# Kernel tuning notes

Measured on AMD Instinct MI355X. Metric: run time of the kernel, lower is better.

## Reference

```python
import jax, jax.numpy as jnp
import numpy as np

B, P, E, H = 32, 16, 50000, 128
EPS = 1e-5


def setup_inputs() -> dict:
    key = jax.random.key(0)
    ks = jax.random.split(key, 8)
    return {
        "inputs": jax.random.randint(ks[0], (B, P, E), 0, 2, dtype=jnp.int32),
        "emb": jax.random.normal(ks[1], (E, H), jnp.float32) * 0.02,
        "w1": jax.random.normal(ks[2], (H, H), jnp.float32) / np.sqrt(H),
        "b1": jax.random.normal(ks[3], (H,), jnp.float32) * 0.01,
        "w2": jax.random.normal(ks[4], (H, H), jnp.float32) / np.sqrt(H),
        "b2": jax.random.normal(ks[5], (H,), jnp.float32) * 0.01,
        "ln1_g": jnp.ones((H,), jnp.float32),
        "ln1_b": jnp.zeros((H,), jnp.float32),
        "ln2_g": jnp.ones((H,), jnp.float32),
        "ln2_b": jnp.zeros((H,), jnp.float32),
        "bn1_g": jnp.ones((H,), jnp.float32),
        "bn1_b": jnp.zeros((H,), jnp.float32),
        "bn2_g": jnp.ones((H,), jnp.float32),
        "bn2_b": jnp.zeros((H,), jnp.float32),
    }


def _layer_norm(x, g, b):
    mu = x.mean(-1, keepdims=True)
    var = ((x - mu) ** 2).mean(-1, keepdims=True)
    return g * (x - mu) / jnp.sqrt(var + EPS) + b


def _batch_norm_eval(x, g, b):
    # eval-mode BatchNorm1d with running_mean=0, running_var=1
    return g * x / jnp.sqrt(1.0 + EPS) + b


def reference(inputs, emb, w1, b1, w2, b2, ln1_g, ln1_b, ln2_g, ln2_b,
              bn1_g, bn1_b, bn2_g, bn2_b):
    # padding_idx=0: embedding row 0 is zero (but still counted in the mean,
    # matching the torch loop which averages over all selected indices)
    emb0 = emb.at[0].set(0.0)
    mask = (inputs == 1).astype(emb.dtype)            # [B, P, E] multi-hot
    sums = jnp.einsum("bpe,eh->bph", mask, emb0)       # segment-sum as one GEMM
    cnt = mask.sum(-1, keepdims=True)                  # [B, P, 1]
    path_emb = jnp.where(cnt > 0, sums / jnp.maximum(cnt, 1.0), 0.0)
    x = path_emb.mean(axis=1)                          # mean over paths -> [B, H]
    x = _layer_norm(x, ln1_g, ln1_b)
    x = jax.nn.relu(x @ w1.T + b1)
    x = _batch_norm_eval(x, bn1_g, bn1_b)              # dropout = identity (eval)
    x = _layer_norm(x, ln2_g, ln2_b)
    x = jax.nn.relu(x @ w2.T + b2)
    x = _batch_norm_eval(x, bn2_g, bn2_b)
    return x
```

## Files before the change

### kernel.cpp

```cpp
#include <hip/hip_runtime.h>
#include <stdint.h>

#define E_DIM 50000
#define EP2   50176
#define HD    128
#define BD    32
#define PD    16
#define MD    512
#define KCHUNK 448
#define NKC   112
#define NST   7
#define NEB   784
#define EPSF  1e-5f

typedef short short8 __attribute__((ext_vector_type(8)));
typedef float f32x4  __attribute__((ext_vector_type(4)));

__device__ __forceinline__ uint16_t f2bf(float f) {
  uint32_t u = __float_as_uint(f);
  u += 0x7FFFu + ((u >> 16) & 1u);
  return (uint16_t)(u >> 16);
}

__global__ __launch_bounds__(256) void k_prep(const float* __restrict__ emb,
                                              const int* __restrict__ inp,
                                              uint16_t* __restrict__ embF,
                                              uint8_t* __restrict__ bitsT,
                                              float* __restrict__ cnt) {
  __shared__ __align__(16) uint16_t lds[HD * 64];
  __shared__ int sc[4];
  const int t = threadIdx.x;

  if (blockIdx.x < NEB) {
    const int e0 = blockIdx.x * 64;
#pragma unroll
    for (int pass = 0; pass < 8; ++pass) {
      const int el = pass * 8 + (t >> 5);
      const int h  = (t & 31) * 4;
      const int eg = e0 + el;
      float4 v = {0.f, 0.f, 0.f, 0.f};
      if (eg < E_DIM && eg != 0)
        v = *(const float4*)(emb + (size_t)eg * HD + h);
      const uint16_t q0 = f2bf(v.x), q1 = f2bf(v.y), q2 = f2bf(v.z), q3 = f2bf(v.w);
      lds[(h + 0) * 64 + (el ^ (((h + 0) & 7) << 3))] = q0;
      lds[(h + 1) * 64 + (el ^ (((h + 1) & 7) << 3))] = q1;
      lds[(h + 2) * 64 + (el ^ (((h + 2) & 7) << 3))] = q2;
      lds[(h + 3) * 64 + (el ^ (((h + 3) & 7) << 3))] = q3;
    }
    __syncthreads();
    const int w    = t >> 6;
    const int lane = t & 63;
    const int r16  = lane & 15;
    const int kgq  = (lane >> 4) * 8;
    uint16_t* outp = embF + (size_t)blockIdx.x * 8192 + lane * 8;
#pragma unroll
    for (int fr = 0; fr < 4; ++fr) {
      const int f  = w * 4 + fr;
      const int h  = (f & 7) * 16 + r16;
      const int el = (f >> 3) * 32 + kgq;
      short8 d = *(const short8*)(lds + h * 64 + (el ^ ((h & 7) << 3)));
      *(short8*)(outp + f * 512) = d;
    }
  } else {
    const int r = blockIdx.x - NEB;
    const int* rp = inp + (size_t)r * E_DIM;
    int c = 0;
#pragma unroll 3
    for (int i = 0; i < 24; ++i) {
      const int idx = i * 2048 + t * 8;
      const int4 v0 = *(const int4*)(rp + idx);
      const int4 v1 = *(const int4*)(rp + idx + 4);
      const uint32_t b = (uint32_t)(v0.x == 1)        | ((uint32_t)(v0.y == 1) << 1)
                       | ((uint32_t)(v0.z == 1) << 2) | ((uint32_t)(v0.w == 1) << 3)
                       | ((uint32_t)(v1.x == 1) << 4) | ((uint32_t)(v1.y == 1) << 5)
                       | ((uint32_t)(v1.z == 1) << 6) | ((uint32_t)(v1.w == 1) << 7);
      c += __popc(b);
      const int c0 = i * 256 + t;
      bitsT[(size_t)(c0 / 56) * 28672 + r * 56 + (c0 % 56)] = (uint8_t)b;
    }
    if (t < 106) {
      const int idx = 49152 + t * 8;
      const int4 v0 = *(const int4*)(rp + idx);
      const int4 v1 = *(const int4*)(rp + idx + 4);
      const uint32_t b = (uint32_t)(v0.x == 1)        | ((uint32_t)(v0.y == 1) << 1)
                       | ((uint32_t)(v0.z == 1) << 2) | ((uint32_t)(v0.w == 1) << 3)
                       | ((uint32_t)(v1.x == 1) << 4) | ((uint32_t)(v1.y == 1) << 5)
                       | ((uint32_t)(v1.z == 1) << 6) | ((uint32_t)(v1.w == 1) << 7);
      c += __popc(b);
      const int c0 = 6144 + t;
      bitsT[(size_t)(c0 / 56) * 28672 + r * 56 + (c0 % 56)] = (uint8_t)b;
    } else if (t < 128) {
      const int c0 = 6144 + t;
      bitsT[(size_t)(c0 / 56) * 28672 + r * 56 + (c0 % 56)] = 0;
    }
#pragma unroll
    for (int o = 1; o < 64; o <<= 1) c += __shfl_xor(c, o);
    if ((t & 63) == 0) sc[t >> 6] = c;
    __syncthreads();
    if (t == 0) cnt[r] = (float)(sc[0] + sc[1] + sc[2] + sc[3]);
  }
}

__global__ __launch_bounds__(512, 4) void k_gemm(const uint8_t* __restrict__ bitsT,
                                                 const uint16_t* __restrict__ embF,
                                                 uint16_t* __restrict__ part) {
  __shared__ __align__(16) uint8_t lds[57344];

  const int t    = threadIdx.x;
  const int lane = t & 63;
  const int w    = t >> 6;
  const int kc   = blockIdx.x >> 2;
  const int ch   = blockIdx.x & 3;

  {
    const char* eb = (const char*)embF + (size_t)kc * 114688;
    const char* ab = (const char*)bitsT + (size_t)kc * 28672;
#define BADDR(IDX) (eb + ((IDX) >> 8) * 16384 + ((((IDX) >> 7) & 1) * 8192) \
                       + ((ch * 2 + (((IDX) >> 6) & 1)) * 1024) + ((IDX) & 63) * 16)
    uint4 b0, b1, b2, b3, a0, a1, a2, a3;
    b0 = *(const uint4*)BADDR(t);
    b1 = *(const uint4*)BADDR(512 + t);
    b2 = *(const uint4*)BADDR(1024 + t);
    a0 = *(const uint4*)(ab + t * 16);
    a1 = *(const uint4*)(ab + (512 + t) * 16);
    a2 = *(const uint4*)(ab + (1024 + t) * 16);
    if (t < 256) {
      b3 = *(const uint4*)BADDR(1536 + t);
      a3 = *(const uint4*)(ab + (1536 + t) * 16);
    }
    *(uint4*)(lds + t * 16)                  = b0;
    *(uint4*)(lds + (512 + t) * 16)          = b1;
    *(uint4*)(lds + (1024 + t) * 16)         = b2;
    *(uint4*)(lds + 28672 + t * 16)          = a0;
    *(uint4*)(lds + 28672 + (512 + t) * 16)  = a1;
    *(uint4*)(lds + 28672 + (1024 + t) * 16) = a2;
    if (t < 256) {
      *(uint4*)(lds + (1536 + t) * 16)          = b3;
      *(uint4*)(lds + 28672 + (1536 + t) * 16)  = a3;
    }
#undef BADDR
  }
  __syncthreads();

  const int r16 = lane & 15;
  const int g4  = lane >> 4;
  const int abase = 28672 + (w * 64 + r16) * 56 + g4;
  const int bbase = lane * 16;

  f32x4 acc[4][2];
#pragma unroll
  for (int rg = 0; rg < 4; ++rg)
#pragma unroll
    for (int cg = 0; cg < 2; ++cg) acc[rg][cg] = (f32x4){0.f, 0.f, 0.f, 0.f};

#define UNPACK(DST, B)                                            \
  {                                                               \
    union { uint32_t u[4]; short8 s; } x_;                        \
    x_.u[0] = ((B) & 1u) * 0x3F80u        + ((B) & 2u) * 0x1FC00000u;   \
    x_.u[1] = (((B) >> 2) & 1u) * 0x3F80u + (((B) >> 2) & 2u) * 0x1FC00000u; \
    x_.u[2] = (((B) >> 4) & 1u) * 0x3F80u + (((B) >> 4) & 2u) * 0x1FC00000u; \
    x_.u[3] = (((B) >> 6) & 1u) * 0x3F80u + (((B) >> 6) & 2u) * 0x1FC00000u; \
    DST = x_.s;                                                   \
  }

#pragma unroll
  for (int s = 0; s < NST; ++s) {
    short8 bf[2][2];
#pragma unroll
    for (int ks = 0; ks < 2; ++ks)
#pragma unroll
      for (int cg = 0; cg < 2; ++cg)
        bf[ks][cg] = *(const short8*)(lds + s * 4096 + ks * 2048 + cg * 1024 + bbase);
#pragma unroll
    for (int rg = 0; rg < 4; ++rg) {
#pragma unroll
      for (int ks = 0; ks < 2; ++ks) {
        const uint32_t b = lds[abase + rg * 896 + s * 8 + ks * 4];
        short8 af;
        UNPACK(af, b)
        acc[rg][0] = __builtin_amdgcn_mfma_f32_16x16x32_bf16(af, bf[ks][0], acc[rg][0], 0, 0, 0);
        acc[rg][1] = __builtin_amdgcn_mfma_f32_16x16x32_bf16(af, bf[ks][1], acc[rg][1], 0, 0, 0);
      }
    }
  }
#undef UNPACK

  const int jr = (lane >> 4) << 2;
#pragma unroll
  for (int rg = 0; rg < 4; ++rg)
#pragma unroll
    for (int cg = 0; cg < 2; ++cg) {
      uint16_t* pt = part + (size_t)kc * (MD * HD)
                   + (size_t)(w * 64 + rg * 16 + jr) * HD + ch * 32 + cg * 16 + r16;
#pragma unroll
      for (int j = 0; j < 4; ++j)
        pt[j * HD] = f2bf(acc[rg][cg][j]);
    }
}

__global__ __launch_bounds__(512) void k_reduce(const uint16_t* __restrict__ part,
                                                const float* __restrict__ cnt,
                                                float* __restrict__ pe) {
  __shared__ float red[512];
  const int r   = blockIdx.x;
  const int t   = threadIdx.x;
  const int col = t & 127;
  const int sub = t >> 7;
  const uint16_t* pp = part + (size_t)(sub * 28) * (MD * HD) + (size_t)r * HD + col;
  float s = 0.f;
#pragma unroll
  for (int i = 0; i < 28; ++i)
    s += __uint_as_float((uint32_t)pp[(size_t)i * (MD * HD)] << 16);
  red[t] = s;
  __syncthreads();
  if (t < 128) {
    const float tot = red[t] + red[t + 128] + red[t + 256] + red[t + 384];
    const float c   = cnt[r];
    pe[r * HD + t] = (c > 0.f) ? (tot / c) : 0.f;
  }
}

__global__ __launch_bounds__(128) void k_tail(
    const float* __restrict__ pe,
    const float* __restrict__ w1, const float* __restrict__ b1,
    const float* __restrict__ w2, const float* __restrict__ b2,
    const float* __restrict__ ln1g, const float* __restrict__ ln1b,
    const float* __restrict__ ln2g, const float* __restrict__ ln2b,
    const float* __restrict__ bn1g, const float* __restrict__ bn1b,
    const float* __restrict__ bn2g, const float* __restrict__ bn2b,
    float* __restrict__ out) {
  const int b = blockIdx.x, t = threadIdx.x;
  __shared__ float sh[HD];
  __shared__ float red[HD];

  float x = 0.f;
#pragma unroll
  for (int p = 0; p < PD; ++p) x += pe[(b * PD + p) * HD + t];
  x *= (1.f / PD);

  const float bninv = rsqrtf(1.f + EPSF);

  red[t] = x; __syncthreads();
  for (int o = 64; o > 0; o >>= 1) { if (t < o) red[t] += red[t + o]; __syncthreads(); }
  const float mu1 = red[0] * (1.f / HD); __syncthreads();
  const float d1 = x - mu1;
  red[t] = d1 * d1; __syncthreads();
  for (int o = 64; o > 0; o >>= 1) { if (t < o) red[t] += red[t + o]; __syncthreads(); }
  const float v1 = red[0] * (1.f / HD); __syncthreads();
  const float y1 = ln1g[t] * d1 * rsqrtf(v1 + EPSF) + ln1b[t];

  sh[t] = y1; __syncthreads();
  float a = b1[t];
  const float4* wrow1 = (const float4*)(w1 + (size_t)t * HD);
#pragma unroll 8
  for (int k = 0; k < 32; ++k) {
    const float4 w = wrow1[k];
    a += w.x * sh[k * 4] + w.y * sh[k * 4 + 1] + w.z * sh[k * 4 + 2] + w.w * sh[k * 4 + 3];
  }
  a = fmaxf(a, 0.f);
  a = bn1g[t] * a * bninv + bn1b[t];
  __syncthreads();

  red[t] = a; __syncthreads();
  for (int o = 64; o > 0; o >>= 1) { if (t < o) red[t] += red[t + o]; __syncthreads(); }
  const float mu2 = red[0] * (1.f / HD); __syncthreads();
  const float d2 = a - mu2;
  red[t] = d2 * d2; __syncthreads();
  for (int o = 64; o > 0; o >>= 1) { if (t < o) red[t] += red[t + o]; __syncthreads(); }
  const float v2 = red[0] * (1.f / HD); __syncthreads();
  const float y2 = ln2g[t] * d2 * rsqrtf(v2 + EPSF) + ln2b[t];

  sh[t] = y2; __syncthreads();
  float a2 = b2[t];
  const float4* wrow2 = (const float4*)(w2 + (size_t)t * HD);
#pragma unroll 8
  for (int k = 0; k < 32; ++k) {
    const float4 w = wrow2[k];
    a2 += w.x * sh[k * 4] + w.y * sh[k * 4 + 1] + w.z * sh[k * 4 + 2] + w.w * sh[k * 4 + 3];
  }
  a2 = fmaxf(a2, 0.f);
  a2 = bn2g[t] * a2 * bninv + bn2b[t];
  out[b * HD + t] = a2;
}

extern "C" void kernel_launch(void* const* d_in, const int* in_sizes, int n_in,
                              void* d_out, int out_size, void* d_ws, size_t ws_size,
                              hipStream_t stream) {
  const int*   inp  = (const int*)d_in[0];
  const float* emb  = (const float*)d_in[1];
  const float* w1   = (const float*)d_in[2];
  const float* b1   = (const float*)d_in[3];
  const float* w2   = (const float*)d_in[4];
  const float* b2   = (const float*)d_in[5];
  const float* ln1g = (const float*)d_in[6];
  const float* ln1b = (const float*)d_in[7];
  const float* ln2g = (const float*)d_in[8];
  const float* ln2b = (const float*)d_in[9];
  const float* bn1g = (const float*)d_in[10];
  const float* bn1b = (const float*)d_in[11];
  const float* bn2g = (const float*)d_in[12];
  const float* bn2b = (const float*)d_in[13];
  float* out = (float*)d_out;

  char* ws = (char*)d_ws;
  uint8_t*  bitsT = (uint8_t*)ws;
  uint16_t* embF  = (uint16_t*)(ws + 3211328);
  uint16_t* part  = (uint16_t*)(ws + 3211328 + 12845056);
  float*    cnt   = (float*)(ws + 3211328 + 12845056 + 14680064);
  float*    pe    = (float*)(ws + 3211328 + 12845056 + 14680064 + 2048);

  k_prep<<<NEB + MD, 256, 0, stream>>>(emb, inp, embF, bitsT, cnt);
  k_gemm<<<NKC * 4, 512, 0, stream>>>(bitsT, embF, part);
  k_reduce<<<MD, 512, 0, stream>>>(part, cnt, pe);
  k_tail<<<BD, 128, 0, stream>>>(pe, w1, b1, w2, b2, ln1g, ln1b, ln2g, ln2b,
                                 bn1g, bn1b, bn2g, bn2b, out);
}
```

Baseline: 61.95 us.

## Fuse prep, GEMM, reduce and tail into one cooperative persistent kernel

Replaces the four separate launches with one cooperative kernel of 256 blocks. The prep, split-K GEMM and reduce/tail phases are separated by grid-wide syncs, and each block handles several prep and GEMM units. The reduce kernel is folded into the tail, so each of 32 blocks sums all K-chunk partials for its 16 rows and no pe buffer is written. The aim is to remove launch gaps and a global round trip, at the cost of grid-sync overhead, fewer blocks in flight, and a serial 112-chunk reduction on only 32 blocks. A fallback to three regular launches covers the case where the cooperative launch fails.

Result: slower. 168.7 us (+172.4%).

```diff
diff --git a/kernel.cpp b/kernel.cpp
--- a/kernel.cpp
+++ b/kernel.cpp
@@ -1,5 +1,8 @@
 #include <hip/hip_runtime.h>
+#include <hip/hip_cooperative_groups.h>
 #include <stdint.h>
+
+namespace cg = cooperative_groups;
 
 #define E_DIM 50000
 #define EP2   50176
@@ -7,10 +10,10 @@
 #define BD    32
 #define PD    16
 #define MD    512
-#define KCHUNK 448
 #define NKC   112
 #define NST   7
 #define NEB   784
+#define GRID  256
 #define EPSF  1e-5f
 
 typedef short short8 __attribute__((ext_vector_type(8)));
@@ -22,95 +25,83 @@
   return (uint16_t)(u >> 16);
 }
 
-__global__ __launch_bounds__(256) void k_prep(const float* __restrict__ emb,
-                                              const int* __restrict__ inp,
-                                              uint16_t* __restrict__ embF,
-                                              uint8_t* __restrict__ bitsT,
-                                              float* __restrict__ cnt) {
-  __shared__ __align__(16) uint16_t lds[HD * 64];
-  __shared__ int sc[4];
-  const int t = threadIdx.x;
-
-  if (blockIdx.x < NEB) {
-    const int e0 = blockIdx.x * 64;
-#pragma unroll
-    for (int pass = 0; pass < 8; ++pass) {
-      const int el = pass * 8 + (t >> 5);
-      const int h  = (t & 31) * 4;
-      const int eg = e0 + el;
-      float4 v = {0.f, 0.f, 0.f, 0.f};
-      if (eg < E_DIM && eg != 0)
-        v = *(const float4*)(emb + (size_t)eg * HD + h);
-      const uint16_t q0 = f2bf(v.x), q1 = f2bf(v.y), q2 = f2bf(v.z), q3 = f2bf(v.w);
-      lds[(h + 0) * 64 + (el ^ (((h + 0) & 7) << 3))] = q0;
-      lds[(h + 1) * 64 + (el ^ (((h + 1) & 7) << 3))] = q1;
-      lds[(h + 2) * 64 + (el ^ (((h + 2) & 7) << 3))] = q2;
-      lds[(h + 3) * 64 + (el ^ (((h + 3) & 7) << 3))] = q3;
-    }
-    __syncthreads();
-    const int w    = t >> 6;
-    const int lane = t & 63;
-    const int r16  = lane & 15;
-    const int kgq  = (lane >> 4) * 8;
-    uint16_t* outp = embF + (size_t)blockIdx.x * 8192 + lane * 8;
-#pragma unroll
-    for (int fr = 0; fr < 4; ++fr) {
-      const int f  = w * 4 + fr;
-      const int h  = (f & 7) * 16 + r16;
-      const int el = (f >> 3) * 32 + kgq;
-      short8 d = *(const short8*)(lds + h * 64 + (el ^ ((h & 7) << 3)));
-      *(short8*)(outp + f * 512) = d;
-    }
-  } else {
-    const int r = blockIdx.x - NEB;
-    const int* rp = inp + (size_t)r * E_DIM;
-    int c = 0;
+
+__device__ __forceinline__ void embF_load(const float* __restrict__ emb,
+                                          int unit, int tt, uint16_t* tl) {
+#pragma unroll
+  for (int pass = 0; pass < 8; ++pass) {
+    const int el = pass * 8 + (tt >> 5);
+    const int h  = (tt & 31) * 4;
+    const int eg = unit * 64 + el;
+    float4 v = {0.f, 0.f, 0.f, 0.f};
+    if (eg < E_DIM && eg != 0)
+      v = *(const float4*)(emb + (size_t)eg * HD + h);
+    const uint16_t q0 = f2bf(v.x), q1 = f2bf(v.y), q2 = f2bf(v.z), q3 = f2bf(v.w);
+    tl[(h + 0) * 64 + (el ^ (((h + 0) & 7) << 3))] = q0;
+    tl[(h + 1) * 64 + (el ^ (((h + 1) & 7) << 3))] = q1;
+    tl[(h + 2) * 64 + (el ^ (((h + 2) & 7) << 3))] = q2;
+    tl[(h + 3) * 64 + (el ^ (((h + 3) & 7) << 3))] = q3;
+  }
+}
+__device__ __forceinline__ void embF_store(uint16_t* __restrict__ embF,
+                                           int unit, int tt, const uint16_t* tl) {
+  const int w = tt >> 6, lane = tt & 63;
+  const int r16 = lane & 15, kgq = (lane >> 4) * 8;
+  uint16_t* outp = embF + (size_t)unit * 8192 + lane * 8;
+#pragma unroll
+  for (int fr = 0; fr < 4; ++fr) {
+    const int f  = w * 4 + fr;
+    const int h  = (f & 7) * 16 + r16;
+    const int el = (f >> 3) * 32 + kgq;
+    short8 d = *(const short8*)(tl + h * 64 + (el ^ ((h & 7) << 3)));
+    *(short8*)(outp + f * 512) = d;
+  }
+}
+
+__device__ __forceinline__ int bitpack_row(const int* __restrict__ inp,
+                                           uint8_t* __restrict__ bitsT,
+                                           int r, int t) {
+  const int* rp = inp + (size_t)r * E_DIM;
+  int c = 0;
 #pragma unroll 3
-    for (int i = 0; i < 24; ++i) {
-      const int idx = i * 2048 + t * 8;
-      const int4 v0 = *(const int4*)(rp + idx);
-      const int4 v1 = *(const int4*)(rp + idx + 4);
-      const uint32_t b = (uint32_t)(v0.x == 1)        | ((uint32_t)(v0.y == 1) << 1)
-                       | ((uint32_t)(v0.z == 1) << 2) | ((uint32_t)(v0.w == 1) << 3)
-                       | ((uint32_t)(v1.x == 1) << 4) | ((uint32_t)(v1.y == 1) << 5)
-                       | ((uint32_t)(v1.z == 1) << 6) | ((uint32_t)(v1.w == 1) << 7);
-      c += __popc(b);
-      const int c0 = i * 256 + t;
-      bitsT[(size_t)(c0 / 56) * 28672 + r * 56 + (c0 % 56)] = (uint8_t)b;
-    }
-    if (t < 106) {
-      const int idx = 49152 + t * 8;
-      const int4 v0 = *(const int4*)(rp + idx);
-      const int4 v1 = *(const int4*)(rp + idx + 4);
-      const uint32_t b = (uint32_t)(v0.x == 1)        | ((uint32_t)(v0.y == 1) << 1)
-                       | ((uint32_t)(v0.z == 1) << 2) | ((uint32_t)(v0.w == 1) << 3)
-                       | ((uint32_t)(v1.x == 1) << 4) | ((uint32_t)(v1.y == 1) << 5)
-                       | ((uint32_t)(v1.z == 1) << 6) | ((uint32_t)(v1.w == 1) << 7);
-      c += __popc(b);
-      const int c0 = 6144 + t;
-      bitsT[(size_t)(c0 / 56) * 28672 + r * 56 + (c0 % 56)] = (uint8_t)b;
-    } else if (t < 128) {
-      const int c0 = 6144 + t;
-      bitsT[(size_t)(c0 / 56) * 28672 + r * 56 + (c0 % 56)] = 0;
-    }
-#pragma unroll
-    for (int o = 1; o < 64; o <<= 1) c += __shfl_xor(c, o);
-    if ((t & 63) == 0) sc[t >> 6] = c;
-    __syncthreads();
-    if (t == 0) cnt[r] = (float)(sc[0] + sc[1] + sc[2] + sc[3]);
-  }
-}
-
-__global__ __launch_bounds__(512, 4) void k_gemm(const uint8_t* __restrict__ bitsT,
-                                                 const uint16_t* __restrict__ embF,
-                                                 uint16_t* __restrict__ part) {
-  __shared__ __align__(16) uint8_t lds[57344];
-
-  const int t    = threadIdx.x;
+  for (int i = 0; i < 12; ++i) {
+    const int idx = i * 4096 + t * 8;
+    const int4 v0 = *(const int4*)(rp + idx);
+    const int4 v1 = *(const int4*)(rp + idx + 4);
+    const uint32_t b = (uint32_t)(v0.x == 1)        | ((uint32_t)(v0.y == 1) << 1)
+                     | ((uint32_t)(v0.z == 1) << 2) | ((uint32_t)(v0.w == 1) << 3)
+                     | ((uint32_t)(v1.x == 1) << 4) | ((uint32_t)(v1.y == 1) << 5)
+                     | ((uint32_t)(v1.z == 1) << 6) | ((uint32_t)(v1.w == 1) << 7);
+    c += __popc(b);
+    const int c0 = i * 512 + t;
+    bitsT[(size_t)(c0 / 56) * 28672 + r * 56 + (c0 % 56)] = (uint8_t)b;
+  }
+  if (t < 106) {
+    const int idx = 49152 + t * 8;
+    const int4 v0 = *(const int4*)(rp + idx);
+    const int4 v1 = *(const int4*)(rp + idx + 4);
+    const uint32_t b = (uint32_t)(v0.x == 1)        | ((uint32_t)(v0.y == 1) << 1)
+                     | ((uint32_t)(v0.z == 1) << 2) | ((uint32_t)(v0.w == 1) << 3)
+                     | ((uint32_t)(v1.x == 1) << 4) | ((uint32_t)(v1.y == 1) << 5)
+                     | ((uint32_t)(v1.z == 1) << 6) | ((uint32_t)(v1.w == 1) << 7);
+    c += __popc(b);
+    const int c0 = 6144 + t;
+    bitsT[(size_t)(c0 / 56) * 28672 + r * 56 + (c0 % 56)] = (uint8_t)b;
+  } else if (t < 128) {
+    const int c0 = 6144 + t;
+    bitsT[(size_t)(c0 / 56) * 28672 + r * 56 + (c0 % 56)] = 0;
+  }
+  return c;
+}
+
+__device__ __forceinline__ void gemm_unit(const uint8_t* __restrict__ bitsT,
+                                          const uint16_t* __restrict__ embF,
+                                          uint16_t* __restrict__ part,
+                                          uint8_t* lds, int unit, int t) {
   const int lane = t & 63;
   const int w    = t >> 6;
-  const int kc   = blockIdx.x >> 2;
-  const int ch   = blockIdx.x & 3;
+  const int kc   = unit >> 2;
+  const int ch   = unit & 3;
 
   {
     const char* eb = (const char*)embF + (size_t)kc * 114688;
@@ -198,30 +189,185 @@
     }
 }
 
-__global__ __launch_bounds__(512) void k_reduce(const uint16_t* __restrict__ part,
-                                                const float* __restrict__ cnt,
-                                                float* __restrict__ pe) {
-  __shared__ float red[512];
-  const int r   = blockIdx.x;
+__device__ __forceinline__ void rt_block(const uint16_t* __restrict__ part,
+    const float* __restrict__ cnt,
+    const float* __restrict__ w1, const float* __restrict__ b1,
+    const float* __restrict__ w2, const float* __restrict__ b2,
+    const float* __restrict__ ln1g, const float* __restrict__ ln1b,
+    const float* __restrict__ ln2g, const float* __restrict__ ln2b,
+    const float* __restrict__ bn1g, const float* __restrict__ bn1b,
+    const float* __restrict__ bn2g, const float* __restrict__ bn2b,
+    float* __restrict__ out, uint8_t* ldsraw, int b, int t) {
+  float* peL = (float*)ldsraw;
+  float* red = (float*)ldsraw + 2048;
+  float* sh  = (float*)ldsraw + 2176;
+
+#pragma unroll
+  for (int i = 0; i < 4; ++i) {
+    const int cell = t + i * 512;
+    const int row = cell >> 7, col = cell & 127;
+    const int r = b * PD + row;
+    const uint16_t* pp = part + (size_t)r * HD + col;
+    float s = 0.f;
+#pragma unroll 4
+    for (int kc = 0; kc < NKC; ++kc)
+      s += __uint_as_float((uint32_t)pp[(size_t)kc * (MD * HD)] << 16);
+    const float c = cnt[r];
+    peL[cell] = (c > 0.f) ? (s / c) : 0.f;
+  }
+  __syncthreads();
+
+  const bool act = (t < 128);
+  float x = 0.f;
+  if (act) {
+#pragma unroll
+    for (int p = 0; p < PD; ++p) x += peL[p * HD + t];
+    x *= (1.f / PD);
+  }
+  const float bninv = rsqrtf(1.f + EPSF);
+
+  if (act) red[t] = x;
+  __syncthreads();
+  for (int o = 64; o > 0; o >>= 1) { if (t < o) red[t] += red[t + o]; __syncthreads(); }
+  const float mu1 = red[0] * (1.f / HD); __syncthreads();
+  const float d1 = x - mu1;
+  if (act) red[t] = d1 * d1;
+  __syncthreads();
+  for (int o = 64; o > 0; o >>= 1) { if (t < o) red[t] += red[t + o]; __syncthreads(); }
+  const float v1 = red[0] * (1.f / HD); __syncthreads();
+
+  if (act) sh[t] = ln1g[t] * d1 * rsqrtf(v1 + EPSF) + ln1b[t];
+  __syncthreads();
+  float a = 0.f;
+  if (act) {
+    a = b1[t];
+    const float4* wrow1 = (const float4*)(w1 + (size_t)t * HD);
+#pragma unroll 8
+    for (int k = 0; k < 32; ++k) {
+      const float4 w = wrow1[k];
+      a += w.x * sh[k * 4] + w.y * sh[k * 4 + 1] + w.z * sh[k * 4 + 2] + w.w * sh[k * 4 + 3];
+    }
+    a = fmaxf(a, 0.f);
+    a = bn1g[t] * a * bninv + bn1b[t];
+  }
+  __syncthreads();
+
+  if (act) red[t] = a;
+  __syncthreads();
+  for (int o = 64; o > 0; o >>= 1) { if (t < o) red[t] += red[t + o]; __syncthreads(); }
+  const float mu2 = red[0] * (1.f / HD); __syncthreads();
+  const float d2 = a - mu2;
+  if (act) red[t] = d2 * d2;
+  __syncthreads();
+  for (int o = 64; o > 0; o >>= 1) { if (t < o) red[t] += red[t + o]; __syncthreads(); }
+  const float v2 = red[0] * (1.f / HD); __syncthreads();
+
+  if (act) sh[t] = ln2g[t] * d2 * rsqrtf(v2 + EPSF) + ln2b[t];
+  __syncthreads();
+  if (act) {
+    float a2 = b2[t];
+    const float4* wrow2 = (const float4*)(w2 + (size_t)t * HD);
+#pragma unroll 8
+    for (int k = 0; k < 32; ++k) {
+      const float4 w = wrow2[k];
+      a2 += w.x * sh[k * 4] + w.y * sh[k * 4 + 1] + w.z * sh[k * 4 + 2] + w.w * sh[k * 4 + 3];
+    }
+    a2 = fmaxf(a2, 0.f);
+    a2 = bn2g[t] * a2 * bninv + bn2b[t];
+    out[b * HD + t] = a2;
+  }
+}
+
+__device__ __forceinline__ void prep_block(const int* __restrict__ inp,
+                                           const float* __restrict__ emb,
+                                           uint8_t* __restrict__ bitsT,
+                                           uint16_t* __restrict__ embF,
+                                           float* __restrict__ cnt,
+                                           uint8_t* lds, int* sc, int bid, int t) {
+  const int team = t >> 8, tt = t & 255;
+  uint16_t* tl = (uint16_t*)(lds + team * 16384);
+  const int slot = bid * 2 + team;
+  embF_load(emb, slot, tt, tl);
+  __syncthreads();
+  embF_store(embF, slot, tt, tl);
+  __syncthreads();
+  if (slot + 512 < NEB) embF_load(emb, slot + 512, tt, tl);
+  __syncthreads();
+  if (slot + 512 < NEB) embF_store(embF, slot + 512, tt, tl);
+
+  for (int rr = 0; rr < 2; ++rr) {
+    const int r = bid * 2 + rr;
+    int c = bitpack_row(inp, bitsT, r, t);
+#pragma unroll
+    for (int o = 1; o < 64; o <<= 1) c += __shfl_xor(c, o);
+    if ((t & 63) == 0) sc[t >> 6] = c;
+    __syncthreads();
+    if (t == 0) {
+      int s = 0;
+#pragma unroll
+      for (int i = 0; i < 8; ++i) s += sc[i];
+      cnt[r] = (float)s;
+    }
+    __syncthreads();
+  }
+}
+
+__device__ __forceinline__ void gemm_block(const uint8_t* __restrict__ bitsT,
+                                           const uint16_t* __restrict__ embF,
+                                           uint16_t* __restrict__ part,
+                                           uint8_t* lds, int bid, int t) {
+  gemm_unit(bitsT, embF, part, lds, bid, t);
+  if (bid + GRID < NKC * 4) {
+    __syncthreads();
+    gemm_unit(bitsT, embF, part, lds, bid + GRID, t);
+  }
+}
+
+__global__ __launch_bounds__(512, 2) void k_all(
+    const int* __restrict__ inp, const float* __restrict__ emb,
+    const float* __restrict__ w1, const float* __restrict__ b1,
+    const float* __restrict__ w2, const float* __restrict__ b2,
+    const float* __restrict__ ln1g, const float* __restrict__ ln1b,
+    const float* __restrict__ ln2g, const float* __restrict__ ln2b,
+    const float* __restrict__ bn1g, const float* __restrict__ bn1b,
+    const float* __restrict__ bn2g, const float* __restrict__ bn2b,
+    uint8_t* __restrict__ bitsT, uint16_t* __restrict__ embF,
+    uint16_t* __restrict__ part, float* __restrict__ cnt,
+    float* __restrict__ out) {
+  __shared__ __align__(16) uint8_t lds[57344];
+  __shared__ int sc[8];
   const int t   = threadIdx.x;
-  const int col = t & 127;
-  const int sub = t >> 7;
-  const uint16_t* pp = part + (size_t)(sub * 28) * (MD * HD) + (size_t)r * HD + col;
-  float s = 0.f;
-#pragma unroll
-  for (int i = 0; i < 28; ++i)
-    s += __uint_as_float((uint32_t)pp[(size_t)i * (MD * HD)] << 16);
-  red[t] = s;
-  __syncthreads();
-  if (t < 128) {
-    const float tot = red[t] + red[t + 128] + red[t + 256] + red[t + 384];
-    const float c   = cnt[r];
-    pe[r * HD + t] = (c > 0.f) ? (tot / c) : 0.f;
-  }
-}
-
-__global__ __launch_bounds__(128) void k_tail(
-    const float* __restrict__ pe,
+  const int bid = blockIdx.x;
+  cg::grid_group grid = cg::this_grid();
+
+  prep_block(inp, emb, bitsT, embF, cnt, lds, sc, bid, t);
+  grid.sync();
+  gemm_block(bitsT, embF, part, lds, bid, t);
+  grid.sync();
+  if (bid < BD)
+    rt_block(part, cnt, w1, b1, w2, b2, ln1g, ln1b, ln2g, ln2b,
+             bn1g, bn1b, bn2g, bn2b, out, lds, bid, t);
+}
+
+__global__ __launch_bounds__(512, 2) void k_p(const int* __restrict__ inp,
+                                              const float* __restrict__ emb,
+                                              uint8_t* __restrict__ bitsT,
+                                              uint16_t* __restrict__ embF,
+                                              float* __restrict__ cnt) {
+  __shared__ __align__(16) uint8_t lds[57344];
+  __shared__ int sc[8];
+  prep_block(inp, emb, bitsT, embF, cnt, lds, sc, blockIdx.x, threadIdx.x);
+}
+
+__global__ __launch_bounds__(512, 2) void k_g(const uint8_t* __restrict__ bitsT,
+                                              const uint16_t* __restrict__ embF,
+                                              uint16_t* __restrict__ part) {
+  __shared__ __align__(16) uint8_t lds[57344];
+  gemm_block(bitsT, embF, part, lds, blockIdx.x, threadIdx.x);
+}
+
+__global__ __launch_bounds__(512, 2) void k_rt(const uint16_t* __restrict__ part,
+    const float* __restrict__ cnt,
     const float* __restrict__ w1, const float* __restrict__ b1,
     const float* __restrict__ w2, const float* __restrict__ b2,
     const float* __restrict__ ln1g, const float* __restrict__ ln1b,
@@ -229,58 +375,9 @@
     const float* __restrict__ bn1g, const float* __restrict__ bn1b,
     const float* __restrict__ bn2g, const float* __restrict__ bn2b,
     float* __restrict__ out) {
-  const int b = blockIdx.x, t = threadIdx.x;
-  __shared__ float sh[HD];
-  __shared__ float red[HD];
-
-  float x = 0.f;
-#pragma unroll
-  for (int p = 0; p < PD; ++p) x += pe[(b * PD + p) * HD + t];
-  x *= (1.f / PD);
-
-  const float bninv = rsqrtf(1.f + EPSF);
-
-  red[t] = x; __syncthreads();
-  for (int o = 64; o > 0; o >>= 1) { if (t < o) red[t] += red[t + o]; __syncthreads(); }
-  const float mu1 = red[0] * (1.f / HD); __syncthreads();
-  const float d1 = x - mu1;
-  red[t] = d1 * d1; __syncthreads();
-  for (int o = 64; o > 0; o >>= 1) { if (t < o) red[t] += red[t + o]; __syncthreads(); }
-  const float v1 = red[0] * (1.f / HD); __syncthreads();
-  const float y1 = ln1g[t] * d1 * rsqrtf(v1 + EPSF) + ln1b[t];
-
-  sh[t] = y1; __syncthreads();
-  float a = b1[t];
-  const float4* wrow1 = (const float4*)(w1 + (size_t)t * HD);
-#pragma unroll 8
-  for (int k = 0; k < 32; ++k) {
-    const float4 w = wrow1[k];
-    a += w.x * sh[k * 4] + w.y * sh[k * 4 + 1] + w.z * sh[k * 4 + 2] + w.w * sh[k * 4 + 3];
-  }
-  a = fmaxf(a, 0.f);
-  a = bn1g[t] * a * bninv + bn1b[t];
-  __syncthreads();
-
-  red[t] = a; __syncthreads();
-  for (int o = 64; o > 0; o >>= 1) { if (t < o) red[t] += red[t + o]; __syncthreads(); }
-  const float mu2 = red[0] * (1.f / HD); __syncthreads();
-  const float d2 = a - mu2;
-  red[t] = d2 * d2; __syncthreads();
-  for (int o = 64; o > 0; o >>= 1) { if (t < o) red[t] += red[t + o]; __syncthreads(); }
-  const float v2 = red[0] * (1.f / HD); __syncthreads();
-  const float y2 = ln2g[t] * d2 * rsqrtf(v2 + EPSF) + ln2b[t];
-
-  sh[t] = y2; __syncthreads();
-  float a2 = b2[t];
-  const float4* wrow2 = (const float4*)(w2 + (size_t)t * HD);
-#pragma unroll 8
-  for (int k = 0; k < 32; ++k) {
-    const float4 w = wrow2[k];
-    a2 += w.x * sh[k * 4] + w.y * sh[k * 4 + 1] + w.z * sh[k * 4 + 2] + w.w * sh[k * 4 + 3];
-  }
-  a2 = fmaxf(a2, 0.f);
-  a2 = bn2g[t] * a2 * bninv + bn2b[t];
-  out[b * HD + t] = a2;
+  __shared__ __align__(16) uint8_t lds[57344];
+  rt_block(part, cnt, w1, b1, w2, b2, ln1g, ln1b, ln2g, ln2b,
+           bn1g, bn1b, bn2g, bn2b, out, lds, blockIdx.x, threadIdx.x);
 }
 
 extern "C" void kernel_launch(void* const* d_in, const int* in_sizes, int n_in,
@@ -307,11 +404,20 @@
   uint16_t* embF  = (uint16_t*)(ws + 3211328);
   uint16_t* part  = (uint16_t*)(ws + 3211328 + 12845056);
   float*    cnt   = (float*)(ws + 3211328 + 12845056 + 14680064);
-  float*    pe    = (float*)(ws + 3211328 + 12845056 + 14680064 + 2048);
-
-  k_prep<<<NEB + MD, 256, 0, stream>>>(emb, inp, embF, bitsT, cnt);
-  k_gemm<<<NKC * 4, 512, 0, stream>>>(bitsT, embF, part);
-  k_reduce<<<MD, 512, 0, stream>>>(part, cnt, pe);
-  k_tail<<<BD, 128, 0, stream>>>(pe, w1, b1, w2, b2, ln1g, ln1b, ln2g, ln2b,
+
+  void* args[] = {
+    (void*)&inp, (void*)&emb, (void*)&w1, (void*)&b1, (void*)&w2, (void*)&b2,
+    (void*)&ln1g, (void*)&ln1b, (void*)&ln2g, (void*)&ln2b,
+    (void*)&bn1g, (void*)&bn1b, (void*)&bn2g, (void*)&bn2b,
+    (void*)&bitsT, (void*)&embF, (void*)&part, (void*)&cnt, (void*)&out
+  };
+  hipError_t err = hipLaunchCooperativeKernel((const void*)k_all, dim3(GRID),
+                                              dim3(512), args, 0, stream);
+  if (err != hipSuccess) {
+    k_p<<<GRID, 512, 0, stream>>>(inp, emb, bitsT, embF, cnt);
+    k_g<<<GRID, 512, 0, stream>>>(bitsT, embF, part);
+    k_rt<<<BD, 512, 0, stream>>>(part, cnt, w1, b1, w2, b2,
+                                 ln1g, ln1b, ln2g, ln2b,
                                  bn1g, bn1b, bn2g, bn2b, out);
-}
+  }
+}
```

## Retile bit-GEMM to 256-wide K chunks and 64-column blocks, vectorize reduce

Applied to the files above, without the earlier changes.

Splits K into 196 chunks of 256 (instead of 112 of 448) and makes each GEMM block cover 64 output columns instead of 32. Each A-byte unpack then feeds four MFMAs instead of two, and A bits are read as 32-bit words with a shift. The bit layout is changed to match, using power-of-two indexing. The reduce kernel now reads 8 bf16 values per load and sums 196 partials across 16 groups. In exchange, the partial buffer nearly doubles in size, which adds write and read traffic between the GEMM and the reduce, and the GEMM grid changes from 448 to 392 blocks.

After: 60.28 us. 1.03x faster.

```diff
diff --git a/kernel.cpp b/kernel.cpp
--- a/kernel.cpp
+++ b/kernel.cpp
@@ -7,9 +7,9 @@
 #define BD    32
 #define PD    16
 #define MD    512
-#define KCHUNK 448
-#define NKC   112
-#define NST   7
+#define KCHUNK 256
+#define NKC   196
+#define NST   4
 #define NEB   784
 #define EPSF  1e-5f
 
@@ -76,7 +76,7 @@
                        | ((uint32_t)(v1.z == 1) << 6) | ((uint32_t)(v1.w == 1) << 7);
       c += __popc(b);
       const int c0 = i * 256 + t;
-      bitsT[(size_t)(c0 / 56) * 28672 + r * 56 + (c0 % 56)] = (uint8_t)b;
+      bitsT[(size_t)(c0 >> 5) * 16384 + r * 32 + (c0 & 31)] = (uint8_t)b;
     }
     if (t < 106) {
       const int idx = 49152 + t * 8;
@@ -88,10 +88,10 @@
                        | ((uint32_t)(v1.z == 1) << 6) | ((uint32_t)(v1.w == 1) << 7);
       c += __popc(b);
       const int c0 = 6144 + t;
-      bitsT[(size_t)(c0 / 56) * 28672 + r * 56 + (c0 % 56)] = (uint8_t)b;
+      bitsT[(size_t)(c0 >> 5) * 16384 + r * 32 + (c0 & 31)] = (uint8_t)b;
     } else if (t < 128) {
       const int c0 = 6144 + t;
-      bitsT[(size_t)(c0 / 56) * 28672 + r * 56 + (c0 % 56)] = 0;
+      bitsT[(size_t)(c0 >> 5) * 16384 + r * 32 + (c0 & 31)] = 0;
     }
 #pragma unroll
     for (int o = 1; o < 64; o <<= 1) c += __shfl_xor(c, o);
@@ -104,54 +104,42 @@
 __global__ __launch_bounds__(512, 4) void k_gemm(const uint8_t* __restrict__ bitsT,
                                                  const uint16_t* __restrict__ embF,
                                                  uint16_t* __restrict__ part) {
-  __shared__ __align__(16) uint8_t lds[57344];
+  __shared__ __align__(16) uint8_t lds[49152];
 
   const int t    = threadIdx.x;
   const int lane = t & 63;
   const int w    = t >> 6;
-  const int kc   = blockIdx.x >> 2;
-  const int ch   = blockIdx.x & 3;
+  const int kc   = blockIdx.x >> 1;
+  const int ch   = blockIdx.x & 1;
 
   {
-    const char* eb = (const char*)embF + (size_t)kc * 114688;
-    const char* ab = (const char*)bitsT + (size_t)kc * 28672;
-#define BADDR(IDX) (eb + ((IDX) >> 8) * 16384 + ((((IDX) >> 7) & 1) * 8192) \
-                       + ((ch * 2 + (((IDX) >> 6) & 1)) * 1024) + ((IDX) & 63) * 16)
-    uint4 b0, b1, b2, b3, a0, a1, a2, a3;
-    b0 = *(const uint4*)BADDR(t);
-    b1 = *(const uint4*)BADDR(512 + t);
-    b2 = *(const uint4*)BADDR(1024 + t);
-    a0 = *(const uint4*)(ab + t * 16);
-    a1 = *(const uint4*)(ab + (512 + t) * 16);
-    a2 = *(const uint4*)(ab + (1024 + t) * 16);
-    if (t < 256) {
-      b3 = *(const uint4*)BADDR(1536 + t);
-      a3 = *(const uint4*)(ab + (1536 + t) * 16);
-    }
-    *(uint4*)(lds + t * 16)                  = b0;
-    *(uint4*)(lds + (512 + t) * 16)          = b1;
-    *(uint4*)(lds + (1024 + t) * 16)         = b2;
-    *(uint4*)(lds + 28672 + t * 16)          = a0;
-    *(uint4*)(lds + 28672 + (512 + t) * 16)  = a1;
-    *(uint4*)(lds + 28672 + (1024 + t) * 16) = a2;
-    if (t < 256) {
-      *(uint4*)(lds + (1536 + t) * 16)          = b3;
-      *(uint4*)(lds + 28672 + (1536 + t) * 16)  = a3;
-    }
-#undef BADDR
+    const char* eb = (const char*)embF;
+    const char* ab = (const char*)bitsT + (size_t)kc * 16384;
+#pragma unroll
+    for (int i = 0; i < 4; ++i) {
+      const int IDX = t + i * 512;
+      const size_t src = (size_t)(kc * 4 + (IDX >> 9)) * 16384
+                       + (size_t)((((IDX >> 8) & 1) * 8) + ch * 4 + ((IDX >> 6) & 3)) * 1024
+                       + (size_t)(IDX & 63) * 16;
+      *(uint4*)(lds + IDX * 16) = *(const uint4*)(eb + src);
+    }
+#pragma unroll
+    for (int i = 0; i < 2; ++i) {
+      const int IDX = t + i * 512;
+      *(uint4*)(lds + 32768 + IDX * 16) = *(const uint4*)(ab + IDX * 16);
+    }
   }
   __syncthreads();
 
-  const int r16 = lane & 15;
-  const int g4  = lane >> 4;
-  const int abase = 28672 + (w * 64 + r16) * 56 + g4;
-  const int bbase = lane * 16;
-
-  f32x4 acc[4][2];
+  const int r16   = lane & 15;
+  const int shamt = (lane >> 4) * 8;
+  const int abase = 32768 + (w * 64 + r16) * 32;
+
+  f32x4 acc[4][4];
 #pragma unroll
   for (int rg = 0; rg < 4; ++rg)
 #pragma unroll
-    for (int cg = 0; cg < 2; ++cg) acc[rg][cg] = (f32x4){0.f, 0.f, 0.f, 0.f};
+    for (int cg = 0; cg < 4; ++cg) acc[rg][cg] = (f32x4){0.f, 0.f, 0.f, 0.f};
 
 #define UNPACK(DST, B)                                            \
   {                                                               \
@@ -165,21 +153,23 @@
 
 #pragma unroll
   for (int s = 0; s < NST; ++s) {
-    short8 bf[2][2];
-#pragma unroll
-    for (int ks = 0; ks < 2; ++ks)
-#pragma unroll
-      for (int cg = 0; cg < 2; ++cg)
-        bf[ks][cg] = *(const short8*)(lds + s * 4096 + ks * 2048 + cg * 1024 + bbase);
-#pragma unroll
-    for (int rg = 0; rg < 4; ++rg) {
-#pragma unroll
-      for (int ks = 0; ks < 2; ++ks) {
-        const uint32_t b = lds[abase + rg * 896 + s * 8 + ks * 4];
+#pragma unroll
+    for (int ks = 0; ks < 2; ++ks) {
+      const uint8_t* bb = lds + s * 8192 + ks * 4096 + lane * 16;
+      const short8 bf0 = *(const short8*)(bb);
+      const short8 bf1 = *(const short8*)(bb + 1024);
+      const short8 bf2 = *(const short8*)(bb + 2048);
+      const short8 bf3 = *(const short8*)(bb + 3072);
+#pragma unroll
+      for (int rg = 0; rg < 4; ++rg) {
+        const uint32_t b32 = *(const uint32_t*)(lds + abase + rg * 512 + s * 8 + ks * 4);
+        const uint32_t b = (b32 >> shamt) & 0xFFu;
         short8 af;
         UNPACK(af, b)
-        acc[rg][0] = __builtin_amdgcn_mfma_f32_16x16x32_bf16(af, bf[ks][0], acc[rg][0], 0, 0, 0);
-        acc[rg][1] = __builtin_amdgcn_mfma_f32_16x16x32_bf16(af, bf[ks][1], acc[rg][1], 0, 0, 0);
+        acc[rg][0] = __builtin_amdgcn_mfma_f32_16x16x32_bf16(af, bf0, acc[rg][0], 0, 0, 0);
+        acc[rg][1] = __builtin_amdgcn_mfma_f32_16x16x32_bf16(af, bf1, acc[rg][1], 0, 0, 0);
+        acc[rg][2] = __builtin_amdgcn_mfma_f32_16x16x32_bf16(af, bf2, acc[rg][2], 0, 0, 0);
+        acc[rg][3] = __builtin_amdgcn_mfma_f32_16x16x32_bf16(af, bf3, acc[rg][3], 0, 0, 0);
       }
     }
   }
@@ -189,33 +179,44 @@
 #pragma unroll
   for (int rg = 0; rg < 4; ++rg)
 #pragma unroll
-    for (int cg = 0; cg < 2; ++cg) {
+    for (int cg = 0; cg < 4; ++cg) {
       uint16_t* pt = part + (size_t)kc * (MD * HD)
-                   + (size_t)(w * 64 + rg * 16 + jr) * HD + ch * 32 + cg * 16 + r16;
+                   + (size_t)(w * 64 + rg * 16 + jr) * HD + ch * 64 + cg * 16 + r16;
 #pragma unroll
       for (int j = 0; j < 4; ++j)
         pt[j * HD] = f2bf(acc[rg][cg][j]);
     }
 }
 
-__global__ __launch_bounds__(512) void k_reduce(const uint16_t* __restrict__ part,
+__global__ __launch_bounds__(256) void k_reduce(const uint16_t* __restrict__ part,
                                                 const float* __restrict__ cnt,
                                                 float* __restrict__ pe) {
-  __shared__ float red[512];
-  const int r   = blockIdx.x;
-  const int t   = threadIdx.x;
-  const int col = t & 127;
-  const int sub = t >> 7;
-  const uint16_t* pp = part + (size_t)(sub * 28) * (MD * HD) + (size_t)r * HD + col;
-  float s = 0.f;
-#pragma unroll
-  for (int i = 0; i < 28; ++i)
-    s += __uint_as_float((uint32_t)pp[(size_t)i * (MD * HD)] << 16);
-  red[t] = s;
+  __shared__ float red[16 * 128];
+  const int r    = blockIdx.x;
+  const int t    = threadIdx.x;
+  const int col8 = t & 15;
+  const int sub  = t >> 4;
+  float s0=0.f,s1=0.f,s2=0.f,s3=0.f,s4=0.f,s5=0.f,s6=0.f,s7=0.f;
+  const uint16_t* pp = part + (size_t)r * HD + col8 * 8;
+  for (int kc = sub; kc < NKC; kc += 16) {
+    const short8 v = *(const short8*)(pp + (size_t)kc * (MD * HD));
+    s0 += __uint_as_float((uint32_t)(uint16_t)v[0] << 16);
+    s1 += __uint_as_float((uint32_t)(uint16_t)v[1] << 16);
+    s2 += __uint_as_float((uint32_t)(uint16_t)v[2] << 16);
+    s3 += __uint_as_float((uint32_t)(uint16_t)v[3] << 16);
+    s4 += __uint_as_float((uint32_t)(uint16_t)v[4] << 16);
+    s5 += __uint_as_float((uint32_t)(uint16_t)v[5] << 16);
+    s6 += __uint_as_float((uint32_t)(uint16_t)v[6] << 16);
+    s7 += __uint_as_float((uint32_t)(uint16_t)v[7] << 16);
+  }
+  float* rd = red + sub * 128 + col8 * 8;
+  rd[0]=s0; rd[1]=s1; rd[2]=s2; rd[3]=s3; rd[4]=s4; rd[5]=s5; rd[6]=s6; rd[7]=s7;
   __syncthreads();
   if (t < 128) {
-    const float tot = red[t] + red[t + 128] + red[t + 256] + red[t + 384];
-    const float c   = cnt[r];
+    float tot = 0.f;
+#pragma unroll
+    for (int k = 0; k < 16; ++k) tot += red[k * 128 + t];
+    const float c = cnt[r];
     pe[r * HD + t] = (c > 0.f) ? (tot / c) : 0.f;
   }
 }
@@ -306,12 +307,12 @@
   uint8_t*  bitsT = (uint8_t*)ws;
   uint16_t* embF  = (uint16_t*)(ws + 3211328);
   uint16_t* part  = (uint16_t*)(ws + 3211328 + 12845056);
-  float*    cnt   = (float*)(ws + 3211328 + 12845056 + 14680064);
-  float*    pe    = (float*)(ws + 3211328 + 12845056 + 14680064 + 2048);
+  float*    cnt   = (float*)(ws + 3211328 + 12845056 + 25690112);
+  float*    pe    = (float*)(ws + 3211328 + 12845056 + 25690112 + 2048);
 
   k_prep<<<NEB + MD, 256, 0, stream>>>(emb, inp, embF, bitsT, cnt);
-  k_gemm<<<NKC * 4, 512, 0, stream>>>(bitsT, embF, part);
-  k_reduce<<<MD, 512, 0, stream>>>(part, cnt, pe);
+  k_gemm<<<NKC * 2, 512, 0, stream>>>(bitsT, embF, part);
+  k_reduce<<<MD, 256, 0, stream>>>(part, cnt, pe);
   k_tail<<<BD, 128, 0, stream>>>(pe, w1, b1, w2, b2, ln1g, ln1b, ln2g, ln2b,
                                  bn1g, bn1b, bn2g, bn2b, out);
 }
```
